# Performance work log

Hardware: AMD Instinct MI355X
Metric: run time of the kernel (lower is better)

Reference implementation:

```python
import jax, jax.numpy as jnp
import numpy as np

K_HOPS = 3
NUM_GRAPHS = 64
GN_EPS = 1e-5


def setup_inputs() -> dict:
    key = jax.random.key(0)
    ks = jax.random.split(key, 6)
    N, E, F = 50000, 625000, 128
    y = jax.random.normal(ks[0], (N, F), dtype=jnp.float32)
    edge_index = jax.random.randint(ks[1], (2, E), 0, N, dtype=jnp.int64)
    edge_weight = jax.random.uniform(ks[2], (E,), dtype=jnp.float32)
    batch = jnp.sort(jax.random.randint(ks[3], (N,), 0, NUM_GRAPHS, dtype=jnp.int64))
    tag_w = jax.random.normal(ks[4], (K_HOPS + 1, F, F), dtype=jnp.float32) * (1.0 / np.sqrt(F))
    tag_b = jnp.zeros((F,), dtype=jnp.float32)
    gn_weight = jnp.ones((F,), dtype=jnp.float32)
    gn_bias = jnp.zeros((F,), dtype=jnp.float32)
    gn_mean_scale = jnp.ones((F,), dtype=jnp.float32)
    return {"y": y, "edge_index": edge_index, "edge_weight": edge_weight,
            "batch": batch, "tag_w": tag_w, "tag_b": tag_b,
            "gn_weight": gn_weight, "gn_bias": gn_bias, "gn_mean_scale": gn_mean_scale}


def reference(y, edge_index, edge_weight, batch, tag_w, tag_b, gn_weight, gn_bias, gn_mean_scale):
    N = y.shape[0]
    src, dst = edge_index[0], edge_index[1]

    # --- TAGConv: symmetric gcn_norm (no self-loops), K hops ---
    deg = jax.ops.segment_sum(edge_weight, dst, num_segments=N)  # [N]
    dinv = jnp.where(deg > 0, jax.lax.rsqrt(jnp.maximum(deg, 1e-30)), 0.0)
    norm = dinv[src] * edge_weight * dinv[dst]  # [E]

    h = y
    out = h @ tag_w[0]
    for k in range(1, K_HOPS + 1):
        # one hop of message passing: gather from src, scatter-sum at dst
        h = jax.ops.segment_sum(norm[:, None] * h[src], dst, num_segments=N)  # [N,F]
        out = out + h @ tag_w[k]
    out = out + tag_b

    # --- GraphNorm over per-graph segments ---
    cnt = jax.ops.segment_sum(jnp.ones((N,), out.dtype), batch, num_segments=NUM_GRAPHS)
    cnt = jnp.maximum(cnt, 1.0)[:, None]  # [G,1]
    mean = jax.ops.segment_sum(out, batch, num_segments=NUM_GRAPHS) / cnt  # [G,F]
    xc = out - gn_mean_scale * mean[batch]
    var = jax.ops.segment_sum(xc * xc, batch, num_segments=NUM_GRAPHS) / cnt  # [G,F]
    hn = gn_weight * xc * jax.lax.rsqrt(var[batch] + GN_EPS) + gn_bias

    # --- activation; dropout is identity in eval mode; residual ---
    h_act = jax.nn.relu(hn)
    return y + h_act
```

## Files before the change

kernel.cpp:

```cpp
#include <hip/hip_runtime.h>

#define F 128
#define GRAPHS 64
#define GN_EPS 1e-5f
#define SCAN_B 256

typedef short short8 __attribute__((ext_vector_type(8)));
typedef float f32x4 __attribute__((ext_vector_type(4)));

__device__ __forceinline__ unsigned short f2b(float f) {
    unsigned u = __float_as_uint(f);
    unsigned r = (u + 0x7fffu + ((u >> 16) & 1u)) >> 16;
    return (unsigned short)r;
}
__device__ __forceinline__ float b2f(unsigned short h) {
    return __uint_as_float(((unsigned)h) << 16);
}

__global__ void prep_kernel(const int* __restrict__ ei, const float* __restrict__ ew,
                            unsigned long long* __restrict__ packed,
                            unsigned short* __restrict__ rank, int E, int ebl,
                            const float4* __restrict__ y, ushort4* __restrict__ hs0,
                            int n4, int fbl,
                            const float* __restrict__ tw, unsigned short* __restrict__ wf) {
    int b = blockIdx.x;
    if (b < ebl) {
        int e = b * 256 + threadIdx.x;
        if (e < E) {
            int dst = ei[E + e];
            unsigned q = (unsigned)(ew[e] * 16777216.0f + 0.5f);
            unsigned long long old =
                atomicAdd(&packed[dst], (1ull << 40) | (unsigned long long)q);
            rank[e] = (unsigned short)(old >> 40);
        }
    } else if (b < ebl + fbl) {
        int i = (b - ebl) * 256 + threadIdx.x;
        if (i < n4) {
            float4 v = y[i];
            hs0[i] = make_ushort4(f2b(v.x), f2b(v.y), f2b(v.z), f2b(v.w));
        }
    } else {
        int i = (b - ebl - fbl) * 256 + threadIdx.x;
        int seg = i >> 14;
        int r = i & 16383;
        int kb = r >> 12;
        int wc = (r >> 11) & 1;
        int nt = (r >> 9) & 3;
        int lane = (r >> 3) & 63;
        int j = i & 7;
        int k = kb * 32 + (lane >> 4) * 8 + j;
        int n = wc * 64 + nt * 16 + (lane & 15);
        wf[i] = f2b(tw[seg * 16384 + k * 128 + n]);
    }
}

__global__ void node_prep_kernel(const unsigned long long* __restrict__ packed,
                                 float* __restrict__ dinv, const int* __restrict__ batch,
                                 int* __restrict__ gstart, int* __restrict__ excl,
                                 int* __restrict__ blockSums, int n) {
    __shared__ int s[SCAN_B];
    int i = blockIdx.x * SCAN_B + threadIdx.x;
    int v = 0;
    if (i < n) {
        unsigned long long p = packed[i];
        v = (int)(p >> 40);
        float d = (float)(p & 0xFFFFFFFFFFull) * 5.9604644775390625e-8f;
        dinv[i] = (d > 0.f) ? rsqrtf(fmaxf(d, 1e-30f)) : 0.f;
        int b = batch[i];
        if (i == 0) {
            for (int g = 0; g <= b; ++g) gstart[g] = 0;
        } else {
            int bp = batch[i - 1];
            for (int g = bp + 1; g <= b; ++g) gstart[g] = i;
        }
        if (i == n - 1) {
            for (int g = b + 1; g <= GRAPHS; ++g) gstart[g] = n;
        }
    }
    s[threadIdx.x] = v;
    __syncthreads();
    for (int off = 1; off < SCAN_B; off <<= 1) {
        int t = (threadIdx.x >= off) ? s[threadIdx.x - off] : 0;
        __syncthreads();
        s[threadIdx.x] += t;
        __syncthreads();
    }
    if (i < n) excl[i] = s[threadIdx.x] - v;
    if (threadIdx.x == SCAN_B - 1) blockSums[blockIdx.x] = s[SCAN_B - 1];
}

__global__ void scan3_kernel(int* __restrict__ offs, const int* __restrict__ blockSums,
                             int n, int total, int nb) {
    __shared__ int s[SCAN_B];
    int t = threadIdx.x;
    int v = (t < nb) ? blockSums[t] : 0;
    s[t] = v;
    __syncthreads();
    for (int off = 1; off < SCAN_B; off <<= 1) {
        int x = (t >= off) ? s[t - off] : 0;
        __syncthreads();
        s[t] += x;
        __syncthreads();
    }
    int pre = (blockIdx.x == 0) ? 0 : s[blockIdx.x - 1];
    int i = blockIdx.x * SCAN_B + t;
    if (i < n) offs[i] += pre;
    if (i == 0) offs[n] = total;
}

__global__ void scatter_kernel(const int* __restrict__ ei, const float* __restrict__ w,
                               const float* __restrict__ dinv, const int* __restrict__ offs,
                               const unsigned short* __restrict__ rank,
                               unsigned* __restrict__ csr, int E) {
    int e = blockIdx.x * blockDim.x + threadIdx.x;
    if (e >= E) return;
    int s = ei[e];
    int d = ei[E + e];
    unsigned v = ((unsigned)s << 16) | (unsigned)f2b(dinv[s] * w[e]);
    csr[offs[d] + (int)rank[e]] = v;
}

__global__ __launch_bounds__(256) void hop_kernel(const unsigned short* __restrict__ hin,
                                                  unsigned short* __restrict__ hout,
                                                  const int* __restrict__ offs,
                                                  const unsigned* __restrict__ csr,
                                                  const float* __restrict__ dinv, int n) {
    int lane = threadIdx.x & 63;
    int node = blockIdx.x * 4 + (threadIdx.x >> 6);
    if (node >= n) return;
    int g = lane >> 4, fl = lane & 15;
    int e0 = offs[node], e1 = offs[node + 1];
    float acc[8] = {};
    for (int j = e0; j < e1; j += 16) {
        int base = j + g * 4;
        int c0 = min(base + 0, e1 - 1), c1 = min(base + 1, e1 - 1);
        int c2 = min(base + 2, e1 - 1), c3 = min(base + 3, e1 - 1);
        unsigned ed0 = csr[c0], ed1 = csr[c1], ed2 = csr[c2], ed3 = csr[c3];
        float w0 = (base + 0 < e1) ? b2f((unsigned short)(ed0 & 0xffffu)) : 0.f;
        float w1 = (base + 1 < e1) ? b2f((unsigned short)(ed1 & 0xffffu)) : 0.f;
        float w2 = (base + 2 < e1) ? b2f((unsigned short)(ed2 & 0xffffu)) : 0.f;
        float w3 = (base + 3 < e1) ? b2f((unsigned short)(ed3 & 0xffffu)) : 0.f;
        short8 h0 = *(const short8*)(hin + (size_t)(ed0 >> 16) * 128 + fl * 8);
        short8 h1 = *(const short8*)(hin + (size_t)(ed1 >> 16) * 128 + fl * 8);
        short8 h2 = *(const short8*)(hin + (size_t)(ed2 >> 16) * 128 + fl * 8);
        short8 h3 = *(const short8*)(hin + (size_t)(ed3 >> 16) * 128 + fl * 8);
        #pragma unroll
        for (int k = 0; k < 8; ++k) {
            acc[k] += w0 * b2f((unsigned short)h0[k]) + w1 * b2f((unsigned short)h1[k]);
            acc[k] += w2 * b2f((unsigned short)h2[k]) + w3 * b2f((unsigned short)h3[k]);
        }
    }
    #pragma unroll
    for (int k = 0; k < 8; ++k) {
        acc[k] += __shfl_xor(acc[k], 16);
        acc[k] += __shfl_xor(acc[k], 32);
    }
    if (lane < 16) {
        float dd = dinv[node];
        short8 o;
        #pragma unroll
        for (int k = 0; k < 8; ++k) o[k] = (short)f2b(acc[k] * dd);
        *(short8*)(hout + (size_t)node * 128 + fl * 8) = o;
    }
}

__global__ __launch_bounds__(256) void gemm_kernel(const unsigned short* __restrict__ hcat,
                                                   const unsigned short* __restrict__ Wf,
                                                   const float* __restrict__ bias,
                                                   float* __restrict__ outb,
                                                   int M, size_t NF) {
    __shared__ unsigned short As[4][4096];
    int lane = threadIdx.x & 63;
    int wid = threadIdx.x >> 6;
    int wr = wid & 1, wc = wid >> 1;
    int quad = lane >> 4, l15 = lane & 15;
    int row0 = blockIdx.x * 64;
    unsigned short* myA = As[wid];
    f32x4 acc[2][4] = {};

    for (int s = 0; s < 4; ++s) {
        const unsigned short* Aseg = hcat + (size_t)s * NF;
        short8 stg[8];
        #pragma unroll
        for (int i = 0; i < 8; ++i) {
            int flat = i * 64 + lane;
            int r = flat >> 4, c = flat & 15;
            stg[i] = *(const short8*)(Aseg + (size_t)(row0 + wr * 32 + r) * 128 + c * 8);
        }
        #pragma unroll
        for (int i = 0; i < 8; ++i) {
            int flat = i * 64 + lane;
            int r = flat >> 4, c = flat & 15;
            *(short8*)&myA[(r * 16 + (c ^ (r & 15))) * 8] = stg[i];
        }
        #pragma unroll
        for (int kb = 0; kb < 4; ++kb) {
            int swz = ((kb * 4 + quad) ^ l15) * 8;
            short8 a0 = *(short8*)&myA[l15 * 128 + swz];
            short8 a1 = *(short8*)&myA[(16 + l15) * 128 + swz];
            const unsigned short* bb = Wf + (size_t)(((s * 4 + kb) * 2 + wc) * 4) * 512 + lane * 8;
            short8 b0 = *(const short8*)(bb + 0 * 512);
            short8 b1 = *(const short8*)(bb + 1 * 512);
            short8 b2 = *(const short8*)(bb + 2 * 512);
            short8 b3 = *(const short8*)(bb + 3 * 512);
            acc[0][0] = __builtin_amdgcn_mfma_f32_16x16x32_bf16(a0, b0, acc[0][0], 0, 0, 0);
            acc[0][1] = __builtin_amdgcn_mfma_f32_16x16x32_bf16(a0, b1, acc[0][1], 0, 0, 0);
            acc[0][2] = __builtin_amdgcn_mfma_f32_16x16x32_bf16(a0, b2, acc[0][2], 0, 0, 0);
            acc[0][3] = __builtin_amdgcn_mfma_f32_16x16x32_bf16(a0, b3, acc[0][3], 0, 0, 0);
            acc[1][0] = __builtin_amdgcn_mfma_f32_16x16x32_bf16(a1, b0, acc[1][0], 0, 0, 0);
            acc[1][1] = __builtin_amdgcn_mfma_f32_16x16x32_bf16(a1, b1, acc[1][1], 0, 0, 0);
            acc[1][2] = __builtin_amdgcn_mfma_f32_16x16x32_bf16(a1, b2, acc[1][2], 0, 0, 0);
            acc[1][3] = __builtin_amdgcn_mfma_f32_16x16x32_bf16(a1, b3, acc[1][3], 0, 0, 0);
        }
    }

    #pragma unroll
    for (int mt = 0; mt < 2; ++mt) {
        #pragma unroll
        for (int r = 0; r < 4; ++r) {
            int row = row0 + wr * 32 + mt * 16 + quad * 4 + r;
            if (row < M) {
                #pragma unroll
                for (int nt = 0; nt < 4; ++nt) {
                    int col = wc * 64 + nt * 16 + l15;
                    outb[(size_t)row * 128 + col] = acc[mt][nt][r] + bias[col];
                }
            }
        }
    }
}

#define STAT_NODES 32
__global__ __launch_bounds__(256) void stats_kernel(const float* __restrict__ out,
                                                    const int* __restrict__ batch,
                                                    float* __restrict__ S1, float* __restrict__ S2,
                                                    int n) {
    int f = threadIdx.x & 127;
    int par = threadIdx.x >> 7;
    int base = blockIdx.x * STAT_NODES;
    int n1 = min(base + STAT_NODES, n);
    int i0 = base + par;
    if (i0 >= n1) return;
    float s1 = 0.f, s2 = 0.f;
    int curg = batch[i0];
    for (int i = i0; i < n1; i += 2) {
        int g = batch[i];
        if (g != curg) {
            atomicAdd(&S1[curg * F + f], s1);
            atomicAdd(&S2[curg * F + f], s2);
            s1 = 0.f; s2 = 0.f; curg = g;
        }
        float v = out[(size_t)i * F + f];
        s1 += v; s2 += v * v;
    }
    atomicAdd(&S1[curg * F + f], s1);
    atomicAdd(&S2[curg * F + f], s2);
}

__global__ void finalize_kernel(const float* __restrict__ S1, const float* __restrict__ S2,
                                const int* __restrict__ gstart, const float* __restrict__ gnw,
                                const float* __restrict__ gms,
                                float* __restrict__ sm, float* __restrict__ Ag, int GF) {
    int i = blockIdx.x * blockDim.x + threadIdx.x;
    if (i >= GF) return;
    int f = i & (F - 1);
    int g = i >> 7;
    float c = fmaxf((float)(gstart[g + 1] - gstart[g]), 1.f);
    float mean = S1[i] / c;
    float e2 = S2[i] / c;
    float s = gms[f];
    float var = e2 - 2.f * s * mean * mean + s * s * mean * mean;
    sm[i] = s * mean;
    Ag[i] = gnw[f] * rsqrtf(var + GN_EPS);
}

__global__ void final_kernel(const ushort4* __restrict__ yb, const float4* __restrict__ out,
                             const int* __restrict__ batch, const float4* __restrict__ sm,
                             const float4* __restrict__ Ag, const float4* __restrict__ gnb,
                             float4* __restrict__ res, int n) {
    int idx = blockIdx.x * blockDim.x + threadIdx.x;
    if (idx >= n * 32) return;
    int node = idx >> 5;
    int q = idx & 31;
    int g = batch[node];
    float4 o = out[idx];
    ushort4 yv4 = yb[idx];
    float4 m = sm[g * 32 + q];
    float4 a = Ag[g * 32 + q];
    float4 b = gnb[q];
    float4 r;
    r.x = b2f(yv4.x) + fmaxf(0.f, (o.x - m.x) * a.x + b.x);
    r.y = b2f(yv4.y) + fmaxf(0.f, (o.y - m.y) * a.y + b.y);
    r.z = b2f(yv4.z) + fmaxf(0.f, (o.z - m.z) * a.z + b.z);
    r.w = b2f(yv4.w) + fmaxf(0.f, (o.w - m.w) * a.w + b.w);
    res[idx] = r;
}

extern "C" void kernel_launch(void* const* d_in, const int* in_sizes, int n_in,
                              void* d_out, int out_size, void* d_ws, size_t ws_size,
                              hipStream_t stream) {
    const float* y     = (const float*)d_in[0];
    const int*   ei    = (const int*)d_in[1];
    const float* ew    = (const float*)d_in[2];
    const int*   batch = (const int*)d_in[3];
    const float* tag_w = (const float*)d_in[4];
    const float* tag_b = (const float*)d_in[5];
    const float* gnw   = (const float*)d_in[6];
    const float* gnb   = (const float*)d_in[7];
    const float* gms   = (const float*)d_in[8];
    float* res = (float*)d_out;

    const int N = in_sizes[0] / F;
    const int E = in_sizes[1] / 2;
    const size_t NF = (size_t)N * F;

    char* p = (char*)d_ws;
    unsigned long long* packed = (unsigned long long*)p; p += (size_t)N * 8;
    float* S1 = (float*)p;       p += (size_t)GRAPHS * F * 4;
    float* S2 = (float*)p;       p += (size_t)GRAPHS * F * 4;
    size_t zeroBytes = (size_t)(p - (char*)d_ws);
    int*   gstart = (int*)p;     p += 512;
    float* dinv = (float*)p;     p += (size_t)N * 4;
    int*   offs = (int*)p;       p += (size_t)(N + 4) * 4;
    int*   blockSums = (int*)p;  p += 4096;
    unsigned short* rank = (unsigned short*)p; p += ((size_t)E * 2 + 15) & ~15ull;
    unsigned* csr = (unsigned*)p; p += (size_t)E * 4;
    unsigned short* Wf = (unsigned short*)p; p += 4 * 128 * 128 * 2;
    unsigned short* hcat = (unsigned short*)p; p += NF * 2 * 4;
    float* outb = (float*)p;     p += NF * 4;
    float* sm = (float*)p;       p += (size_t)GRAPHS * F * 4;
    float* Ag = (float*)p;       p += (size_t)GRAPHS * F * 4;

    hipMemsetAsync(d_ws, 0, zeroBytes, stream);

    int eb = (E + 255) / 256;
    int sb = (N + SCAN_B - 1) / SCAN_B;
    int n4 = N * 32;
    int fb = (n4 + 255) / 256;
    int wb = (4 * 128 * 128) / 256;

    unsigned short* hs0 = hcat;
    unsigned short* hs1 = hcat + NF;
    unsigned short* hs2 = hcat + 2 * NF;
    unsigned short* hs3 = hcat + 3 * NF;

    prep_kernel<<<eb + fb + wb, 256, 0, stream>>>(ei, ew, packed, rank, E, eb,
                                                  (const float4*)y, (ushort4*)hs0, n4, fb,
                                                  tag_w, Wf);
    node_prep_kernel<<<sb, SCAN_B, 0, stream>>>(packed, dinv, batch, gstart, offs, blockSums, N);
    scan3_kernel<<<sb, SCAN_B, 0, stream>>>(offs, blockSums, N, E, sb);
    scatter_kernel<<<eb, 256, 0, stream>>>(ei, ew, dinv, offs, rank, csr, E);

    int hb = (N + 3) / 4;
    hop_kernel<<<hb, 256, 0, stream>>>(hs0, hs1, offs, csr, dinv, N);
    hop_kernel<<<hb, 256, 0, stream>>>(hs1, hs2, offs, csr, dinv, N);
    hop_kernel<<<hb, 256, 0, stream>>>(hs2, hs3, offs, csr, dinv, N);

    gemm_kernel<<<(N + 63) / 64, 256, 0, stream>>>(hcat, Wf, tag_b, outb, N, NF);

    stats_kernel<<<(N + STAT_NODES - 1) / STAT_NODES, 256, 0, stream>>>(outb, batch, S1, S2, N);
    finalize_kernel<<<(GRAPHS * F + 255) / 256, 256, 0, stream>>>(S1, S2, gstart, gnw, gms, sm, Ag, GRAPHS * F);
    final_kernel<<<(N * 32 + 255) / 256, 256, 0, stream>>>((const ushort4*)hs0, (const float4*)outb,
                                                           batch, (const float4*)sm, (const float4*)Ag,
                                                           (const float4*)gnb, (float4*)res, N);
}
```

Before: 255.3 us.

## Fuse GraphNorm statistics into GEMM epilogue and store GEMM output as bf16

The GEMM epilogue now accumulates per-graph sum and sum-of-squares through shared-memory atomics, with a global-atomic fallback, and writes the GEMM output as bf16 instead of fp32. The separate stats and finalize kernels are removed. The final kernel now computes mean, variance and scale inline from S1/S2. This cuts two launches and a full fp32 read/write pass over the N×F output, at the cost of bf16 rounding of the pre-norm activations and many shared atomics in the epilogue.

```diff
diff --git a/kernel.cpp b/kernel.cpp
--- a/kernel.cpp
+++ b/kernel.cpp
@@ -167,9 +167,12 @@
 __global__ __launch_bounds__(256) void gemm_kernel(const unsigned short* __restrict__ hcat,
                                                    const unsigned short* __restrict__ Wf,
                                                    const float* __restrict__ bias,
-                                                   float* __restrict__ outb,
+                                                   const int* __restrict__ batch,
+                                                   unsigned short* __restrict__ outb,
+                                                   float* __restrict__ S1, float* __restrict__ S2,
                                                    int M, size_t NF) {
     __shared__ unsigned short As[4][4096];
+    __shared__ float sstat[4][2][128];
     int lane = threadIdx.x & 63;
     int wid = threadIdx.x >> 6;
     int wr = wid & 1, wc = wid >> 1;
@@ -177,6 +180,8 @@
     int row0 = blockIdx.x * 64;
     unsigned short* myA = As[wid];
     f32x4 acc[2][4] = {};
+
+    for (int i = threadIdx.x; i < 1024; i += 256) ((float*)sstat)[i] = 0.f;
 
     for (int s = 0; s < 4; ++s) {
         const unsigned short* Aseg = hcat + (size_t)s * NF;
@@ -214,85 +219,90 @@
         }
     }
 
+    __syncthreads();
+    int g0 = batch[row0];
+    float bcol[4];
+    #pragma unroll
+    for (int nt = 0; nt < 4; ++nt) bcol[nt] = bias[wc * 64 + nt * 16 + l15];
+
     #pragma unroll
     for (int mt = 0; mt < 2; ++mt) {
         #pragma unroll
         for (int r = 0; r < 4; ++r) {
             int row = row0 + wr * 32 + mt * 16 + quad * 4 + r;
             if (row < M) {
+                int d = batch[row] - g0;
                 #pragma unroll
                 for (int nt = 0; nt < 4; ++nt) {
                     int col = wc * 64 + nt * 16 + l15;
-                    outb[(size_t)row * 128 + col] = acc[mt][nt][r] + bias[col];
+                    float v = acc[mt][nt][r] + bcol[nt];
+                    outb[(size_t)row * 128 + col] = f2b(v);
+                    if (d < 4) {
+                        atomicAdd(&sstat[d][0][col], v);
+                        atomicAdd(&sstat[d][1][col], v * v);
+                    } else {
+                        atomicAdd(&S1[(size_t)(g0 + d) * 128 + col], v);
+                        atomicAdd(&S2[(size_t)(g0 + d) * 128 + col], v * v);
+                    }
                 }
             }
         }
     }
-}
-
-#define STAT_NODES 32
-__global__ __launch_bounds__(256) void stats_kernel(const float* __restrict__ out,
-                                                    const int* __restrict__ batch,
-                                                    float* __restrict__ S1, float* __restrict__ S2,
-                                                    int n) {
-    int f = threadIdx.x & 127;
-    int par = threadIdx.x >> 7;
-    int base = blockIdx.x * STAT_NODES;
-    int n1 = min(base + STAT_NODES, n);
-    int i0 = base + par;
-    if (i0 >= n1) return;
-    float s1 = 0.f, s2 = 0.f;
-    int curg = batch[i0];
-    for (int i = i0; i < n1; i += 2) {
-        int g = batch[i];
-        if (g != curg) {
-            atomicAdd(&S1[curg * F + f], s1);
-            atomicAdd(&S2[curg * F + f], s2);
-            s1 = 0.f; s2 = 0.f; curg = g;
-        }
-        float v = out[(size_t)i * F + f];
-        s1 += v; s2 += v * v;
-    }
-    atomicAdd(&S1[curg * F + f], s1);
-    atomicAdd(&S2[curg * F + f], s2);
-}
-
-__global__ void finalize_kernel(const float* __restrict__ S1, const float* __restrict__ S2,
-                                const int* __restrict__ gstart, const float* __restrict__ gnw,
-                                const float* __restrict__ gms,
-                                float* __restrict__ sm, float* __restrict__ Ag, int GF) {
-    int i = blockIdx.x * blockDim.x + threadIdx.x;
-    if (i >= GF) return;
-    int f = i & (F - 1);
-    int g = i >> 7;
-    float c = fmaxf((float)(gstart[g + 1] - gstart[g]), 1.f);
-    float mean = S1[i] / c;
-    float e2 = S2[i] / c;
-    float s = gms[f];
-    float var = e2 - 2.f * s * mean * mean + s * s * mean * mean;
-    sm[i] = s * mean;
-    Ag[i] = gnw[f] * rsqrtf(var + GN_EPS);
-}
-
-__global__ void final_kernel(const ushort4* __restrict__ yb, const float4* __restrict__ out,
-                             const int* __restrict__ batch, const float4* __restrict__ sm,
-                             const float4* __restrict__ Ag, const float4* __restrict__ gnb,
+    __syncthreads();
+    int span = batch[min(row0 + 63, M - 1)] - g0;
+    int lim = (min(span, 3) + 1) * 128;
+    for (int i = threadIdx.x; i < lim; i += 256) {
+        int d = i >> 7, c = i & 127;
+        atomicAdd(&S1[(size_t)(g0 + d) * 128 + c], sstat[d][0][c]);
+        atomicAdd(&S2[(size_t)(g0 + d) * 128 + c], sstat[d][1][c]);
+    }
+}
+
+__global__ void final_kernel(const ushort4* __restrict__ yb, const ushort4* __restrict__ ob,
+                             const int* __restrict__ batch, const float* __restrict__ S1,
+                             const float* __restrict__ S2, const int* __restrict__ gstart,
+                             const float* __restrict__ gnw, const float* __restrict__ gnb,
+                             const float* __restrict__ gms,
                              float4* __restrict__ res, int n) {
     int idx = blockIdx.x * blockDim.x + threadIdx.x;
     if (idx >= n * 32) return;
     int node = idx >> 5;
     int q = idx & 31;
     int g = batch[node];
-    float4 o = out[idx];
-    ushort4 yv4 = yb[idx];
-    float4 m = sm[g * 32 + q];
-    float4 a = Ag[g * 32 + q];
-    float4 b = gnb[q];
+    float rc = 1.f / fmaxf((float)(gstart[g + 1] - gstart[g]), 1.f);
+    int base = g * 128 + q * 4;
+    float4 s1 = *(const float4*)&S1[base];
+    float4 s2 = *(const float4*)&S2[base];
+    float4 w  = *(const float4*)&gnw[q * 4];
+    float4 bb = *(const float4*)&gnb[q * 4];
+    float4 sc = *(const float4*)&gms[q * 4];
+    ushort4 yv = yb[idx];
+    ushort4 ov = ob[idx];
     float4 r;
-    r.x = b2f(yv4.x) + fmaxf(0.f, (o.x - m.x) * a.x + b.x);
-    r.y = b2f(yv4.y) + fmaxf(0.f, (o.y - m.y) * a.y + b.y);
-    r.z = b2f(yv4.z) + fmaxf(0.f, (o.z - m.z) * a.z + b.z);
-    r.w = b2f(yv4.w) + fmaxf(0.f, (o.w - m.w) * a.w + b.w);
+    {
+        float m = s1.x * rc, e2 = s2.x * rc, s = sc.x;
+        float var = e2 - (2.f * s - s * s) * m * m;
+        float A = w.x * rsqrtf(var + GN_EPS);
+        r.x = b2f(yv.x) + fmaxf(0.f, (b2f(ov.x) - s * m) * A + bb.x);
+    }
+    {
+        float m = s1.y * rc, e2 = s2.y * rc, s = sc.y;
+        float var = e2 - (2.f * s - s * s) * m * m;
+        float A = w.y * rsqrtf(var + GN_EPS);
+        r.y = b2f(yv.y) + fmaxf(0.f, (b2f(ov.y) - s * m) * A + bb.y);
+    }
+    {
+        float m = s1.z * rc, e2 = s2.z * rc, s = sc.z;
+        float var = e2 - (2.f * s - s * s) * m * m;
+        float A = w.z * rsqrtf(var + GN_EPS);
+        r.z = b2f(yv.z) + fmaxf(0.f, (b2f(ov.z) - s * m) * A + bb.z);
+    }
+    {
+        float m = s1.w * rc, e2 = s2.w * rc, s = sc.w;
+        float var = e2 - (2.f * s - s * s) * m * m;
+        float A = w.w * rsqrtf(var + GN_EPS);
+        r.w = b2f(yv.w) + fmaxf(0.f, (b2f(ov.w) - s * m) * A + bb.w);
+    }
     res[idx] = r;
 }
 
@@ -327,9 +337,8 @@
     unsigned* csr = (unsigned*)p; p += (size_t)E * 4;
     unsigned short* Wf = (unsigned short*)p; p += 4 * 128 * 128 * 2;
     unsigned short* hcat = (unsigned short*)p; p += NF * 2 * 4;
-    float* outb = (float*)p;     p += NF * 4;
-    float* sm = (float*)p;       p += (size_t)GRAPHS * F * 4;
-    float* Ag = (float*)p;       p += (size_t)GRAPHS * F * 4;
+    unsigned short* outb = (unsigned short*)p; p += NF * 2;
+    p += 4096;
 
     hipMemsetAsync(d_ws, 0, zeroBytes, stream);
 
@@ -356,11 +365,9 @@
     hop_kernel<<<hb, 256, 0, stream>>>(hs1, hs2, offs, csr, dinv, N);
     hop_kernel<<<hb, 256, 0, stream>>>(hs2, hs3, offs, csr, dinv, N);
 
-    gemm_kernel<<<(N + 63) / 64, 256, 0, stream>>>(hcat, Wf, tag_b, outb, N, NF);
-
-    stats_kernel<<<(N + STAT_NODES - 1) / STAT_NODES, 256, 0, stream>>>(outb, batch, S1, S2, N);
-    finalize_kernel<<<(GRAPHS * F + 255) / 256, 256, 0, stream>>>(S1, S2, gstart, gnw, gms, sm, Ag, GRAPHS * F);
-    final_kernel<<<(N * 32 + 255) / 256, 256, 0, stream>>>((const ushort4*)hs0, (const float4*)outb,
-                                                           batch, (const float4*)sm, (const float4*)Ag,
-                                                           (const float4*)gnb, (float4*)res, N);
-}
+    gemm_kernel<<<(N + 63) / 64, 256, 0, stream>>>(hcat, Wf, tag_b, batch, outb, S1, S2, N, NF);
+
+    final_kernel<<<(N * 32 + 255) / 256, 256, 0, stream>>>((const ushort4*)hs0, (const ushort4*)outb,
+                                                           batch, S1, S2, gstart, gnw, gnb, gms,
+                                                           (float4*)res, N);
+}
```

New measurement: 318.3 us. 24.7% more time.
